# Kernel tuning notes

Measured on AMD Instinct MI355X. Metric: run time of the kernel, lower is better.

## Reference

```python
import jax, jax.numpy as jnp
import numpy as np

N_NODES = 50000
N_EDGES = 800000
D = 128            # input_dim
H = D // 2         # MLP hidden = input_dim // 2
DO = 2 * D         # MLP output = 2 * input_dim


def setup_inputs() -> dict:
    key = jax.random.key(0)
    k = jax.random.split(key, 8)
    x = jax.random.normal(k[0], (N_NODES, D), dtype=jnp.float32)
    edge_index = jax.random.randint(k[1], (2, N_EDGES), 0, N_NODES, dtype=jnp.int64)
    edge_attr = jax.random.normal(k[2], (N_EDGES, D), dtype=jnp.float32)
    # GINEConv params (train_eps=True -> eps initialized to 0)
    eps = jnp.zeros((), dtype=jnp.float32)
    s1 = 1.0 / np.sqrt(D)
    s2 = 1.0 / np.sqrt(H)
    W1 = jax.random.uniform(k[3], (D, H), minval=-s1, maxval=s1, dtype=jnp.float32)
    b1 = jax.random.uniform(k[4], (H,), minval=-s1, maxval=s1, dtype=jnp.float32)
    W2 = jax.random.uniform(k[5], (H, DO), minval=-s2, maxval=s2, dtype=jnp.float32)
    b2 = jax.random.uniform(k[6], (DO,), minval=-s2, maxval=s2, dtype=jnp.float32)
    return {"x": x, "edge_index": edge_index, "edge_attr": edge_attr,
            "eps": eps, "W1": W1, "b1": b1, "W2": W2, "b2": b2}


def reference(x, edge_index, edge_attr, eps, W1, b1, W2, b2):
    src = edge_index[0]  # message sources (x_j)
    dst = edge_index[1]  # aggregation targets
    # GINE message: ReLU(x_j + e_ij), scatter-sum to target nodes
    msg = jax.nn.relu(x[src] + edge_attr)                       # [E, D]
    agg = jax.ops.segment_sum(msg, dst, num_segments=N_NODES)   # [N, D]
    h = (1.0 + eps) * x + agg                                   # GIN update
    # MLP: Linear -> ReLU -> Linear
    h = jax.nn.relu(h @ W1 + b1)                                # [N, H]
    out = h @ W2 + b2                                           # [N, 2D]
    # outer ReLU applied in GNNModule.forward
    return jax.nn.relu(out)
```

## Files before the change

### kernel.cpp

```cpp
#include <hip/hip_runtime.h>


#define D_IN   128
#define H_DIM  64
#define DO_DIM 256

__global__ __launch_bounds__(256) void hist_kernel(
    const int* __restrict__ ei, int* __restrict__ counts, int E)
{
    int g = blockIdx.x * blockDim.x + threadIdx.x;
    if (g < E) atomicAdd(&counts[ei[E + g]], 1);
}

__global__ __launch_bounds__(1024) void scan_kernel(
    int* __restrict__ counts,
    int* __restrict__ offsets,
    int N)
{
    __shared__ int part[1024];
    const int tid = threadIdx.x;
    const int CH  = (N + 1023) / 1024;
    const int lo  = tid * CH;
    const int hi  = min(lo + CH, N);

    int s = 0;
    for (int i = lo; i < hi; ++i) s += counts[i];
    part[tid] = s;
    __syncthreads();
    for (int off = 1; off < 1024; off <<= 1) {
        int v = (tid >= off) ? part[tid - off] : 0;
        __syncthreads();
        part[tid] += v;
        __syncthreads();
    }
    int run = part[tid] - s;
    for (int i = lo; i < hi; ++i) {
        int c = counts[i];
        offsets[i] = run;
        counts[i]  = run;
        run += c;
    }
    if (tid == 1023) offsets[N] = part[1023];
}

__global__ __launch_bounds__(256) void scatter_kernel(
    const int* __restrict__ ei, int* __restrict__ cursor,
    int2* __restrict__ sorted, int E)
{
    int g = blockIdx.x * blockDim.x + threadIdx.x;
    if (g >= E) return;
    int s = ei[g];
    int d = ei[E + g];
    int pos = atomicAdd(&cursor[d], 1);
    sorted[pos] = make_int2(s, g);
}

__global__ __launch_bounds__(512) void agg_kernel(
    const float* __restrict__ x,
    const float* __restrict__ ea,
    const int*  __restrict__ offsets,
    const int2* __restrict__ sorted,
    const float* __restrict__ epsp,
    float* __restrict__ h,
    int N)
{
    const int gid  = blockIdx.x * blockDim.x + threadIdx.x;
    const int node = gid >> 6;
    const int lane = gid & 63;
    if (node >= N) return;

    const int beg = offsets[node];
    const int end = offsets[node + 1];

    float2 acc = {0.0f, 0.0f};
    for (int e = beg; e < end; ++e) {
        int2 se = sorted[e];
        const float2 xv = *reinterpret_cast<const float2*>(x  + (size_t)se.x * D_IN + lane * 2);
        const float2 av = *reinterpret_cast<const float2*>(ea + (size_t)se.y * D_IN + lane * 2);
        acc.x += fmaxf(xv.x + av.x, 0.0f);
        acc.y += fmaxf(xv.y + av.y, 0.0f);
    }
    const float eps1 = 1.0f + epsp[0];
    const float2 xn = *reinterpret_cast<const float2*>(x + (size_t)node * D_IN + lane * 2);
    float2 hv;
    hv.x = fmaf(eps1, xn.x, acc.x);
    hv.y = fmaf(eps1, xn.y, acc.y);
    *reinterpret_cast<float2*>(h + (size_t)node * D_IN + lane * 2) = hv;
}

#define SH_LD  132
#define SHID_LD 68

__global__ __launch_bounds__(256, 1) void mlp_kernel(
    const float* __restrict__ h,
    const float* __restrict__ W1,
    const float* __restrict__ b1,
    const float* __restrict__ W2,
    const float* __restrict__ b2,
    float* __restrict__ out,
    int N)
{
    __shared__ float sW1[D_IN * H_DIM];
    __shared__ float sW2[H_DIM * DO_DIM];
    __shared__ float sh[64 * SH_LD];
    __shared__ float shid[64 * SHID_LD];
    __shared__ float sb1[H_DIM];
    __shared__ float sb2[DO_DIM];

    const int tid = threadIdx.x;

    for (int i = tid; i < (D_IN * H_DIM) / 4; i += 256)
        reinterpret_cast<float4*>(sW1)[i] = reinterpret_cast<const float4*>(W1)[i];
    for (int i = tid; i < (H_DIM * DO_DIM) / 4; i += 256)
        reinterpret_cast<float4*>(sW2)[i] = reinterpret_cast<const float4*>(W2)[i];
    if (tid < H_DIM) sb1[tid] = b1[tid];
    sb2[tid] = b2[tid];

    const int n0 = blockIdx.x * 64;

    for (int idx = tid; idx < 64 * 32; idx += 256) {
        int n = idx >> 5;
        int f = (idx & 31) * 4;
        int gn = n0 + n;
        float4 v = (gn < N) ? *reinterpret_cast<const float4*>(h + (size_t)gn * D_IN + f)
                            : make_float4(0.f, 0.f, 0.f, 0.f);
        *reinterpret_cast<float4*>(&sh[n * SH_LD + f]) = v;
    }
    __syncthreads();

    const int tx = tid & 15;
    const int ty = tid >> 4;

    {
        float acc[4][4];
        #pragma unroll
        for (int i = 0; i < 4; ++i)
            #pragma unroll
            for (int j = 0; j < 4; ++j)
                acc[i][j] = sb1[tx * 4 + j];

        #pragma unroll 4
        for (int k = 0; k < D_IN; ++k) {
            float4 w = *reinterpret_cast<const float4*>(&sW1[k * H_DIM + tx * 4]);
            #pragma unroll
            for (int i = 0; i < 4; ++i) {
                float hv = sh[(ty * 4 + i) * SH_LD + k];
                acc[i][0] = fmaf(hv, w.x, acc[i][0]);
                acc[i][1] = fmaf(hv, w.y, acc[i][1]);
                acc[i][2] = fmaf(hv, w.z, acc[i][2]);
                acc[i][3] = fmaf(hv, w.w, acc[i][3]);
            }
        }
        #pragma unroll
        for (int i = 0; i < 4; ++i) {
            float4 r;
            r.x = fmaxf(acc[i][0], 0.f);
            r.y = fmaxf(acc[i][1], 0.f);
            r.z = fmaxf(acc[i][2], 0.f);
            r.w = fmaxf(acc[i][3], 0.f);
            *reinterpret_cast<float4*>(&shid[(ty * 4 + i) * SHID_LD + tx * 4]) = r;
        }
    }
    __syncthreads();

    {
        float4 o[4][4];
        #pragma unroll
        for (int i = 0; i < 4; ++i)
            #pragma unroll
            for (int jj = 0; jj < 4; ++jj)
                o[i][jj] = *reinterpret_cast<const float4*>(&sb2[jj * 64 + tx * 4]);

        #pragma unroll 4
        for (int k = 0; k < H_DIM; ++k) {
            float4 w[4];
            #pragma unroll
            for (int jj = 0; jj < 4; ++jj)
                w[jj] = *reinterpret_cast<const float4*>(&sW2[k * DO_DIM + jj * 64 + tx * 4]);
            #pragma unroll
            for (int i = 0; i < 4; ++i) {
                float hv = shid[(ty * 4 + i) * SHID_LD + k];
                #pragma unroll
                for (int jj = 0; jj < 4; ++jj) {
                    o[i][jj].x = fmaf(hv, w[jj].x, o[i][jj].x);
                    o[i][jj].y = fmaf(hv, w[jj].y, o[i][jj].y);
                    o[i][jj].z = fmaf(hv, w[jj].z, o[i][jj].z);
                    o[i][jj].w = fmaf(hv, w[jj].w, o[i][jj].w);
                }
            }
        }
        #pragma unroll
        for (int i = 0; i < 4; ++i) {
            int gn = n0 + ty * 4 + i;
            if (gn < N) {
                #pragma unroll
                for (int jj = 0; jj < 4; ++jj) {
                    float4 r;
                    r.x = fmaxf(o[i][jj].x, 0.f);
                    r.y = fmaxf(o[i][jj].y, 0.f);
                    r.z = fmaxf(o[i][jj].z, 0.f);
                    r.w = fmaxf(o[i][jj].w, 0.f);
                    *reinterpret_cast<float4*>(&out[(size_t)gn * DO_DIM + jj * 64 + tx * 4]) = r;
                }
            }
        }
    }
}

extern "C" void kernel_launch(void* const* d_in, const int* in_sizes, int n_in,
                              void* d_out, int out_size, void* d_ws, size_t ws_size,
                              hipStream_t stream)
{
    const float* x   = (const float*)d_in[0];
    const int*   ei  = (const int*)  d_in[1];
    const float* ea  = (const float*)d_in[2];
    const float* eps = (const float*)d_in[3];
    const float* W1  = (const float*)d_in[4];
    const float* b1  = (const float*)d_in[5];
    const float* W2  = (const float*)d_in[6];
    const float* b2  = (const float*)d_in[7];
    float* out = (float*)d_out;

    const int N = in_sizes[0] / D_IN;
    const int E = in_sizes[1] / 2;

    char* base = (char*)d_ws;
    float* h       = (float*)base;
    size_t off_h   = (size_t)N * D_IN * sizeof(float);
    int*   offsets = (int*)(base + off_h);
    int*   cursor  = offsets + (N + 1);
    size_t off_s   = off_h + (size_t)(2 * N + 1) * sizeof(int);
    off_s = (off_s + 7) & ~(size_t)7;
    int2*  sorted  = (int2*)(base + off_s);

    hipMemsetAsync(cursor, 0, (size_t)N * sizeof(int), stream);

    hist_kernel<<<(E + 255) / 256, 256, 0, stream>>>(ei, cursor, E);
    scan_kernel<<<1, 1024, 0, stream>>>(cursor, offsets, N);
    scatter_kernel<<<(E + 255) / 256, 256, 0, stream>>>(ei, cursor, sorted, E);

    {
        int blocks = (N * 64 + 511) / 512;
        agg_kernel<<<blocks, 512, 0, stream>>>(x, ea, offsets, sorted, eps, h, N);
    }
    {
        int blocks = (N + 63) / 64;
        mlp_kernel<<<blocks, 256, 0, stream>>>(h, W1, b1, W2, b2, out, N);
    }
}
```

Baseline: 914.1 us.

## Vectorize CSR build, pipeline edge index loads, drop MLP weight staging

```diff
diff --git a/kernel.cpp b/kernel.cpp
--- a/kernel.cpp
+++ b/kernel.cpp
@@ -5,11 +5,23 @@
 #define H_DIM  64
 #define DO_DIM 256
 
+typedef float v2f __attribute__((ext_vector_type(2)));
+typedef int   v4i __attribute__((ext_vector_type(4)));
+
 __global__ __launch_bounds__(256) void hist_kernel(
     const int* __restrict__ ei, int* __restrict__ counts, int E)
 {
     int g = blockIdx.x * blockDim.x + threadIdx.x;
-    if (g < E) atomicAdd(&counts[ei[E + g]], 1);
+    int base = g * 4;
+    if (base + 4 <= E) {
+        int4 d = *reinterpret_cast<const int4*>(ei + E + base);
+        atomicAdd(&counts[d.x], 1);
+        atomicAdd(&counts[d.y], 1);
+        atomicAdd(&counts[d.z], 1);
+        atomicAdd(&counts[d.w], 1);
+    } else {
+        for (int i = base; i < E; ++i) atomicAdd(&counts[ei[E + i]], 1);
+    }
 }
 
 __global__ __launch_bounds__(1024) void scan_kernel(
@@ -48,18 +60,27 @@
     int2* __restrict__ sorted, int E)
 {
     int g = blockIdx.x * blockDim.x + threadIdx.x;
-    if (g >= E) return;
-    int s = ei[g];
-    int d = ei[E + g];
-    int pos = atomicAdd(&cursor[d], 1);
-    sorted[pos] = make_int2(s, g);
+    int base = g * 4;
+    if (base + 4 <= E) {
+        int4 s = *reinterpret_cast<const int4*>(ei + base);
+        int4 d = *reinterpret_cast<const int4*>(ei + E + base);
+        int p0 = atomicAdd(&cursor[d.x], 1); sorted[p0] = make_int2(s.x, base + 0);
+        int p1 = atomicAdd(&cursor[d.y], 1); sorted[p1] = make_int2(s.y, base + 1);
+        int p2 = atomicAdd(&cursor[d.z], 1); sorted[p2] = make_int2(s.z, base + 2);
+        int p3 = atomicAdd(&cursor[d.w], 1); sorted[p3] = make_int2(s.w, base + 3);
+    } else {
+        for (int i = base; i < E; ++i) {
+            int pos = atomicAdd(&cursor[ei[E + i]], 1);
+            sorted[pos] = make_int2(ei[i], i);
+        }
+    }
 }
 
 __global__ __launch_bounds__(512) void agg_kernel(
     const float* __restrict__ x,
     const float* __restrict__ ea,
     const int*  __restrict__ offsets,
-    const int2* __restrict__ sorted,
+    const int*  __restrict__ sorted_raw,
     const float* __restrict__ epsp,
     float* __restrict__ h,
     int N)
@@ -69,29 +90,64 @@
     const int lane = gid & 63;
     if (node >= N) return;
 
-    const int beg = offsets[node];
+    int beg       = offsets[node];
     const int end = offsets[node + 1];
 
-    float2 acc = {0.0f, 0.0f};
-    for (int e = beg; e < end; ++e) {
-        int2 se = sorted[e];
-        const float2 xv = *reinterpret_cast<const float2*>(x  + (size_t)se.x * D_IN + lane * 2);
-        const float2 av = *reinterpret_cast<const float2*>(ea + (size_t)se.y * D_IN + lane * 2);
+    const float* xb = x  + lane * 2;
+    const float* eb = ea + lane * 2;
+
+    v2f acc = {0.0f, 0.0f};
+
+    if ((beg & 1) && beg < end) {
+        int src = sorted_raw[beg * 2];
+        int eid = sorted_raw[beg * 2 + 1];
+        v2f xv = *reinterpret_cast<const v2f*>(xb + (size_t)src * D_IN);
+        v2f av = __builtin_nontemporal_load(reinterpret_cast<const v2f*>(eb + (size_t)eid * D_IN));
         acc.x += fmaxf(xv.x + av.x, 0.0f);
         acc.y += fmaxf(xv.y + av.y, 0.0f);
-    }
+        ++beg;
+    }
+
+    int e = beg;
+    if (e + 2 <= end) {
+        v4i cur = __builtin_nontemporal_load(reinterpret_cast<const v4i*>(sorted_raw + e * 2));
+        for (;;) {
+            const int en = e + 2;
+            const bool more = (en + 2 <= end);
+            v4i nxt;
+            if (more) nxt = __builtin_nontemporal_load(reinterpret_cast<const v4i*>(sorted_raw + en * 2));
+            v2f x0 = *reinterpret_cast<const v2f*>(xb + (size_t)cur.x * D_IN);
+            v2f a0 = __builtin_nontemporal_load(reinterpret_cast<const v2f*>(eb + (size_t)cur.y * D_IN));
+            v2f x1 = *reinterpret_cast<const v2f*>(xb + (size_t)cur.z * D_IN);
+            v2f a1 = __builtin_nontemporal_load(reinterpret_cast<const v2f*>(eb + (size_t)cur.w * D_IN));
+            acc.x += fmaxf(x0.x + a0.x, 0.0f) + fmaxf(x1.x + a1.x, 0.0f);
+            acc.y += fmaxf(x0.y + a0.y, 0.0f) + fmaxf(x1.y + a1.y, 0.0f);
+            e = en;
+            if (!more) break;
+            cur = nxt;
+        }
+    }
+    if (e < end) {
+        int src = sorted_raw[e * 2];
+        int eid = sorted_raw[e * 2 + 1];
+        v2f xv = *reinterpret_cast<const v2f*>(xb + (size_t)src * D_IN);
+        v2f av = __builtin_nontemporal_load(reinterpret_cast<const v2f*>(eb + (size_t)eid * D_IN));
+        acc.x += fmaxf(xv.x + av.x, 0.0f);
+        acc.y += fmaxf(xv.y + av.y, 0.0f);
+    }
+
     const float eps1 = 1.0f + epsp[0];
-    const float2 xn = *reinterpret_cast<const float2*>(x + (size_t)node * D_IN + lane * 2);
-    float2 hv;
+    v2f xn = *reinterpret_cast<const v2f*>(xb + (size_t)node * D_IN);
+    v2f hv;
     hv.x = fmaf(eps1, xn.x, acc.x);
     hv.y = fmaf(eps1, xn.y, acc.y);
-    *reinterpret_cast<float2*>(h + (size_t)node * D_IN + lane * 2) = hv;
-}
-
-#define SH_LD  132
+    *reinterpret_cast<v2f*>(h + (size_t)node * D_IN + lane * 2) = hv;
+}
+
+#define SH_LD   132
 #define SHID_LD 68
 
-__global__ __launch_bounds__(256, 1) void mlp_kernel(
+__global__ __launch_bounds__(256, 3) void mlp_kernel(
     const float* __restrict__ h,
     const float* __restrict__ W1,
     const float* __restrict__ b1,
@@ -100,22 +156,10 @@
     float* __restrict__ out,
     int N)
 {
-    __shared__ float sW1[D_IN * H_DIM];
-    __shared__ float sW2[H_DIM * DO_DIM];
     __shared__ float sh[64 * SH_LD];
     __shared__ float shid[64 * SHID_LD];
-    __shared__ float sb1[H_DIM];
-    __shared__ float sb2[DO_DIM];
 
     const int tid = threadIdx.x;
-
-    for (int i = tid; i < (D_IN * H_DIM) / 4; i += 256)
-        reinterpret_cast<float4*>(sW1)[i] = reinterpret_cast<const float4*>(W1)[i];
-    for (int i = tid; i < (H_DIM * DO_DIM) / 4; i += 256)
-        reinterpret_cast<float4*>(sW2)[i] = reinterpret_cast<const float4*>(W2)[i];
-    if (tid < H_DIM) sb1[tid] = b1[tid];
-    sb2[tid] = b2[tid];
-
     const int n0 = blockIdx.x * 64;
 
     for (int idx = tid; idx < 64 * 32; idx += 256) {
@@ -132,16 +176,15 @@
     const int ty = tid >> 4;
 
     {
+        float4 bv = *reinterpret_cast<const float4*>(b1 + tx * 4);
         float acc[4][4];
         #pragma unroll
-        for (int i = 0; i < 4; ++i)
-            #pragma unroll
-            for (int j = 0; j < 4; ++j)
-                acc[i][j] = sb1[tx * 4 + j];
-
+        for (int i = 0; i < 4; ++i) {
+            acc[i][0] = bv.x; acc[i][1] = bv.y; acc[i][2] = bv.z; acc[i][3] = bv.w;
+        }
         #pragma unroll 4
         for (int k = 0; k < D_IN; ++k) {
-            float4 w = *reinterpret_cast<const float4*>(&sW1[k * H_DIM + tx * 4]);
+            float4 w = *reinterpret_cast<const float4*>(W1 + k * H_DIM + tx * 4);
             #pragma unroll
             for (int i = 0; i < 4; ++i) {
                 float hv = sh[(ty * 4 + i) * SH_LD + k];
@@ -166,17 +209,17 @@
     {
         float4 o[4][4];
         #pragma unroll
-        for (int i = 0; i < 4; ++i)
-            #pragma unroll
-            for (int jj = 0; jj < 4; ++jj)
-                o[i][jj] = *reinterpret_cast<const float4*>(&sb2[jj * 64 + tx * 4]);
-
-        #pragma unroll 4
+        for (int jj = 0; jj < 4; ++jj) {
+            float4 bv = *reinterpret_cast<const float4*>(b2 + jj * 64 + tx * 4);
+            #pragma unroll
+            for (int i = 0; i < 4; ++i) o[i][jj] = bv;
+        }
+        #pragma unroll 2
         for (int k = 0; k < H_DIM; ++k) {
             float4 w[4];
             #pragma unroll
             for (int jj = 0; jj < 4; ++jj)
-                w[jj] = *reinterpret_cast<const float4*>(&sW2[k * DO_DIM + jj * 64 + tx * 4]);
+                w[jj] = *reinterpret_cast<const float4*>(W2 + k * DO_DIM + jj * 64 + tx * 4);
             #pragma unroll
             for (int i = 0; i < 4; ++i) {
                 float hv = shid[(ty * 4 + i) * SHID_LD + k];
@@ -230,18 +273,18 @@
     int*   offsets = (int*)(base + off_h);
     int*   cursor  = offsets + (N + 1);
     size_t off_s   = off_h + (size_t)(2 * N + 1) * sizeof(int);
-    off_s = (off_s + 7) & ~(size_t)7;
+    off_s = (off_s + 15) & ~(size_t)15;
     int2*  sorted  = (int2*)(base + off_s);
 
     hipMemsetAsync(cursor, 0, (size_t)N * sizeof(int), stream);
 
-    hist_kernel<<<(E + 255) / 256, 256, 0, stream>>>(ei, cursor, E);
+    hist_kernel<<<(E / 4 + 255) / 256, 256, 0, stream>>>(ei, cursor, E);
     scan_kernel<<<1, 1024, 0, stream>>>(cursor, offsets, N);
-    scatter_kernel<<<(E + 255) / 256, 256, 0, stream>>>(ei, cursor, sorted, E);
+    scatter_kernel<<<(E / 4 + 255) / 256, 256, 0, stream>>>(ei, cursor, sorted, E);
 
     {
         int blocks = (N * 64 + 511) / 512;
-        agg_kernel<<<blocks, 512, 0, stream>>>(x, ea, offsets, sorted, eps, h, N);
+        agg_kernel<<<blocks, 512, 0, stream>>>(x, ea, offsets, (const int*)sorted, eps, h, N);
     }
     {
         int blocks = (N + 63) / 64;
```

New measurement: 865.7 us. 5.3% less time.
